# Kernel optimization log

Measured on AMD Instinct MI355X. Metric: run time of the kernel, lower is better.

## Reference

```python
import jax, jax.numpy as jnp
import numpy as np

C_IN, SEQ_LEN, K, G = 12, 8192, 8, 64
DIVISOR = 2 if G > 1 else 1
_G = G // DIVISOR
MAX_EXP = int(np.log2((SEQ_LEN - 1) / (9 - 1)))
DILATIONS = [2 ** e for e in range(MAX_EXP + 1)]   # 10 dilations for seq_len=8192
PADDINGS = [(9 - 1) * d // 2 for d in DILATIONS]
C_IN_PER = int(np.clip(C_IN // 2, 2, 8))
BATCH = 32


def _normalize(W):
    # zero-mean, L1-normalized over the kernel taps (last dim)
    W = W - W.mean(-1, keepdims=True)
    return W / jnp.abs(W).sum(-1, keepdims=True)


def setup_inputs() -> dict:
    key = jax.random.key(0)
    kx, kw, ki = jax.random.split(key, 3)
    X = jax.random.normal(kx, (BATCH, C_IN, SEQ_LEN), dtype=jnp.float32)
    # W: (num_dilations, divisor, k*_g, 1, 9) grouped-conv kernels
    W = _normalize(jax.random.normal(kw, (len(DILATIONS), DIVISOR, K * _G, 1, 9), dtype=jnp.float32))
    # I: (num_dilations, divisor, _g, c_in_per) channel-gather indices
    I = jax.random.randint(ki, (len(DILATIONS), DIVISOR, _G, C_IN_PER), 0, C_IN)
    return {"X": X, "W": W, "I": I}


def _branch(inp, Wd, d, p):
    # inp: (bs, _G, L); Wd: (K*_G, 1, 9); grouped dilated conv, 1 in-ch -> K out-ch per group
    z = jax.lax.conv_general_dilated(
        inp, Wd, window_strides=(1,), padding=[(p, p)], rhs_dilation=(d,),
        dimension_numbers=("NCH", "OIH", "NCH"), feature_group_count=_G)
    bs = inp.shape[0]
    z = z.reshape(bs, _G, K, -1)                      # (bs, _G, K, L)
    max_vals = z.max(axis=2)                          # (bs, _G, L)
    max_idx = z.argmax(axis=2)
    min_idx = z.argmin(axis=2)
    # histogram over K bins: sum of max values at argmax bin; count at argmin bin
    cmax = jnp.stack([jnp.where(max_idx == i, max_vals, 0.0).sum(-1) for i in range(K)], axis=-1)
    cmin = jnp.stack([(min_idx == i).astype(inp.dtype).sum(-1) for i in range(K)], axis=-1)
    return cmax, cmin                                 # each (bs, _G, K)


def reference(X, W, I):
    diff_X = jnp.diff(X, axis=-1)
    Z = []
    for di, (d, p) in enumerate(zip(DILATIONS, PADDINGS)):
        for j in range(min(2, G)):
            src = X if j == 0 else diff_X
            inp = src[:, I[di, j]].sum(2)             # gather channels, sum -> (bs, _G, L)
            cmax, cmin = _branch(inp, W[di, j], d, p)
            Z.append(cmax)
            Z.append(cmin)
    Z = jnp.concatenate(Z, axis=1)                    # (bs, 4*num_dilations*_G, K)
    return jax.nn.relu(Z)
```

## Files before the change

kernel.cpp:

```cpp
#include <hip/hip_runtime.h>


typedef __fp16 h2_t __attribute__((ext_vector_type(2)));

#define NB    32
#define CIN   12
#define SEQ   8192
#define NG    32
#define CPER  6
#define OUTCH 1280
#define XS_FLOATS 7728
#define GRID  10240

#define MAX3F(a, b, c) ({ float _r; asm("v_max3_f32 %0, %1, %2, %3" \
    : "=v"(_r) : "v"(a), "v"(b), "v"(c)); _r; })
#define MIN3F(a, b, c) ({ float _r; asm("v_min3_f32 %0, %1, %2, %3" \
    : "=v"(_r) : "v"(a), "v"(b), "v"(c)); _r; })

template <int DI>
__device__ __forceinline__ void hydra_body(
    const float* __restrict__ X, const float* __restrict__ W,
    const int* __restrict__ I, float* __restrict__ out,
    float* Xs, float* Smx, int j, int b, int chunk) {

  constexpr int d   = 1 << DI;
  constexpr int R   = (d < 16) ? d : 16;
  constexpr int rb  = (DI < 4) ? DI : 4;
  constexpr int Mm  = SEQ / d;
  constexpr int TMc = 512 / R;
  constexpr int TM  = (TMc < Mm) ? TMc : Mm;
  constexpr int MC  = Mm / TM;
  constexpr int RC  = d / R;
  constexpr int NR  = (RC * MC) / 16;
  constexpr int SR  = TM + 8;
  constexpr int CS  = R * SR + 4;
  constexpr int CL  = (R >= 8) ? TM : (TM * R / 8);
  constexpr int REP = (R == 16) ? 2 : 1;

  const int L = SEQ - j;
  const int tid = threadIdx.x;
  const int g = tid >> 3, s = tid & 7;

  h2_t Wp[8][4];
  float Wt[8];
  {
    const float* wp = W + (size_t)((DI * 2 + j) * 256 + g * 8) * 9;
#pragma unroll
    for (int k = 0; k < 8; ++k) {
#pragma unroll
      for (int t = 0; t < 4; ++t)
        Wp[k][t] = __builtin_amdgcn_cvt_pkrtz(wp[k * 9 + 2 * t], wp[k * 9 + 2 * t + 1]);
      Wt[k] = wp[k * 9 + 8];
    }
  }
  const float* base[CPER];
  {
    const int* ip = I + ((DI * 2 + j) * NG + g) * CPER;
#pragma unroll
    for (int i = 0; i < CPER; ++i) base[i] = Xs + ip[i] * CS;
  }

#pragma unroll
  for (int k = 0; k < 8; ++k) Smx[k * 256 + tid] = 0.f;

  unsigned long long cmnp = 0ull;

  for (int n = 0; n < NR; ++n) {
    const int cidx = chunk + 16 * n;
    const int rc = cidx & (RC - 1);
    const int mc = cidx / RC;
    const int r0 = rc * R;
    const int m0 = mc * TM;

    if (NR > 1 && n) __syncthreads();

    {
      const float* xb0 = X + (size_t)b * CIN * SEQ;
      if (j == 0) {
        for (int f = tid; f < R * SR; f += 256) {
          int rr = f & (R - 1), mm = f >> rb, mp = m0 + mm - 4;
          int pos = r0 + rr + mp * d;
          bool ok = (mp >= 0) && (pos < L);
          int lo = rr * SR + mm;
          const float* xp = xb0 + pos;
#pragma unroll
          for (int ch = 0; ch < CIN; ++ch) {
            Xs[ch * CS + lo] = ok ? xp[0] : 0.f;
            xp += SEQ;
          }
        }
      } else {
        for (int f = tid; f < R * SR; f += 256) {
          int rr = f & (R - 1), mm = f >> rb, mp = m0 + mm - 4;
          int pos = r0 + rr + mp * d;
          bool ok = (mp >= 0) && (pos < L);
          int lo = rr * SR + mm;
          const float* xp = xb0 + pos;
#pragma unroll
          for (int ch = 0; ch < CIN; ++ch) {
            Xs[ch * CS + lo] = ok ? (xp[1] - xp[0]) : 0.f;
            xp += SEQ;
          }
        }
      }
    }
    __syncthreads();

#pragma unroll
    for (int rep = 0; rep < REP; ++rep) {
      int rr = (R == 16) ? (s + (rep << 3)) : (s & (R - 1));
      int mst = (R >= 8) ? 0 : ((s >> rb) * CL);
      int rowoff = rr * SR + mst;

      auto ldsum = [&](int idx) {
        float4 r = *reinterpret_cast<const float4*>(base[0] + idx);
#pragma unroll
        for (int i = 1; i < CPER; ++i) {
          float4 t = *reinterpret_cast<const float4*>(base[i] + idx);
          r.x += t.x; r.y += t.y; r.z += t.z; r.w += t.w;
        }
        return r;
      };

      float4 w0 = ldsum(rowoff);
      float4 w1 = ldsum(rowoff + 4);
#pragma unroll 1
      for (int st = 0; st < CL; st += 8) {
        float4 w2 = ldsum(rowoff + st + 8);
        float4 w3 = ldsum(rowoff + st + 12);
        float xv[16] = {w0.x, w0.y, w0.z, w0.w,
                        w1.x, w1.y, w1.z, w1.w,
                        w2.x, w2.y, w2.z, w2.w,
                        w3.x, w3.y, w3.z, w3.w};
        h2_t E[8], O[7];
#pragma unroll
        for (int i = 0; i < 8; ++i)
          E[i] = __builtin_amdgcn_cvt_pkrtz(xv[2 * i], xv[2 * i + 1]);
#pragma unroll
        for (int i = 0; i < 7; ++i)
          O[i] = __builtin_amdgcn_cvt_pkrtz(xv[2 * i + 1], xv[2 * i + 2]);
#pragma unroll
        for (int p = 0; p < 8; ++p) {
          const h2_t* P = (p & 1) ? (O + (p >> 1)) : (E + (p >> 1));
          float tail = xv[8 + p];
          float zp[8];
#pragma unroll
          for (int k = 0; k < 8; ++k) {
            float acc = Wt[k] * tail;
            acc = __builtin_amdgcn_fdot2(Wp[k][3], P[3], acc, false);
            acc = __builtin_amdgcn_fdot2(Wp[k][2], P[2], acc, false);
            acc = __builtin_amdgcn_fdot2(Wp[k][1], P[1], acc, false);
            acc = __builtin_amdgcn_fdot2(Wp[k][0], P[0], acc, false);
            zp[k] = __uint_as_float((__float_as_uint(acc) & 0xFFFFFFF8u) | (unsigned)k);
          }
          float t1 = MAX3F(zp[0], zp[1], zp[2]);
          float t2 = MAX3F(zp[3], zp[4], zp[5]);
          float t3 = MAX3F(zp[6], zp[7], t1);
          float mxp = fmaxf(t2, t3);
          float u1 = MIN3F(zp[0], zp[1], zp[2]);
          float u2 = MIN3F(zp[3], zp[4], zp[5]);
          float u3 = MIN3F(zp[6], zp[7], u1);
          float mnp = fminf(u2, u3);
          unsigned mxb = __float_as_uint(mxp);
          Smx[((mxb & 7u) << 8) + tid] += mxp;
          unsigned mnb = __float_as_uint(mnp);
          cmnp += 1ull << ((mnb & 7u) << 3);
        }
        w0 = w2; w1 = w3;
      }
    }
  }

  __syncthreads();

  {
    int cbase = (DI * 2 + j) * 64;
    float sum = 0.f;
#pragma unroll
    for (int s2 = 0; s2 < 8; ++s2) sum += Smx[(s << 8) + (g << 3) + s2];
    atomicAdd(out + ((size_t)b * OUTCH + cbase + g) * 8 + s, sum);

    int cnts[8];
#pragma unroll
    for (int k = 0; k < 8; ++k) cnts[k] = (int)((cmnp >> (k * 8)) & 0xFFull);
#pragma unroll
    for (int k = 0; k < 8; ++k) {
#pragma unroll
      for (int off = 1; off < 8; off <<= 1)
        cnts[k] += __shfl_xor(cnts[k], off);
    }
    int vn = cnts[0];
#pragma unroll
    for (int k = 1; k < 8; ++k) vn = (s == k) ? cnts[k] : vn;
    atomicAdd(out + ((size_t)b * OUTCH + cbase + 32 + g) * 8 + s, (float)vn);
  }
}

__global__ __launch_bounds__(256, 3) void hydra_fused(
    const float* __restrict__ X, const float* __restrict__ W,
    const int* __restrict__ I, float* __restrict__ out) {
  __shared__ float Xs[XS_FLOATS];
  __shared__ float Smx[2048];
  int u = blockIdx.x;
  int dj = u % 20;
  int rest = u / 20;
  int b = rest & 31;
  int chunk = rest >> 5;
  int j = dj & 1;
  switch (dj >> 1) {
    case 0: hydra_body<0>(X, W, I, out, Xs, Smx, j, b, chunk); break;
    case 1: hydra_body<1>(X, W, I, out, Xs, Smx, j, b, chunk); break;
    case 2: hydra_body<2>(X, W, I, out, Xs, Smx, j, b, chunk); break;
    case 3: hydra_body<3>(X, W, I, out, Xs, Smx, j, b, chunk); break;
    case 4: hydra_body<4>(X, W, I, out, Xs, Smx, j, b, chunk); break;
    case 5: hydra_body<5>(X, W, I, out, Xs, Smx, j, b, chunk); break;
    case 6: hydra_body<6>(X, W, I, out, Xs, Smx, j, b, chunk); break;
    case 7: hydra_body<7>(X, W, I, out, Xs, Smx, j, b, chunk); break;
    case 8: hydra_body<8>(X, W, I, out, Xs, Smx, j, b, chunk); break;
    case 9: hydra_body<9>(X, W, I, out, Xs, Smx, j, b, chunk); break;
  }
}

__global__ void hydra_relu(float* __restrict__ out, int n) {
  int i = blockIdx.x * 256 + threadIdx.x;
  if (i < n) out[i] = fmaxf(out[i], 0.f);
}

extern "C" void kernel_launch(void* const* d_in, const int* in_sizes, int n_in,
                              void* d_out, int out_size, void* d_ws, size_t ws_size,
                              hipStream_t stream) {
  const float* X = (const float*)d_in[0];
  const float* W = (const float*)d_in[1];
  const int*   I = (const int*)d_in[2];
  float* out = (float*)d_out;

  (void)hipMemsetAsync(d_out, 0, (size_t)out_size * sizeof(float), stream);
  hydra_fused<<<GRID, 256, 0, stream>>>(X, W, I, out);
  hydra_relu<<<(out_size + 255) / 256, 256, 0, stream>>>(out, out_size);
}
```

Baseline: 421.5 us.

## Stage inputs in fp16 shared memory and fold the ninth tap into fdot2

The shared-memory staging buffer now holds fp16 values instead of fp32. Each thread converts and writes two positions at once as a packed half pair, and the channel gather-sum is done with 8-wide half vector adds. Even/odd packed pairs come from bit shifts instead of cvt_pkrtz, and the ninth tap becomes a fifth fdot2 with a zero-padded weight. The aim is to halve LDS footprint and traffic, drop conversion instructions, and allow more blocks per CU (launch bounds raised from 3 to 5). The channel sum is now accumulated in fp16, which loses more precision than the fp32 sum it replaces.

```diff
diff --git a/kernel.cpp b/kernel.cpp
--- a/kernel.cpp
+++ b/kernel.cpp
@@ -2,6 +2,7 @@
 
 
 typedef __fp16 h2_t __attribute__((ext_vector_type(2)));
+typedef __fp16 h8_t __attribute__((ext_vector_type(8)));
 
 #define NB    32
 #define CIN   12
@@ -9,7 +10,7 @@
 #define NG    32
 #define CPER  6
 #define OUTCH 1280
-#define XS_FLOATS 7728
+#define XS_H  7776
 #define GRID  10240
 
 #define MAX3F(a, b, c) ({ float _r; asm("v_max3_f32 %0, %1, %2, %3" \
@@ -21,7 +22,7 @@
 __device__ __forceinline__ void hydra_body(
     const float* __restrict__ X, const float* __restrict__ W,
     const int* __restrict__ I, float* __restrict__ out,
-    float* Xs, float* Smx, int j, int b, int chunk) {
+    __fp16* Xs, float* Smx, int j, int b, int chunk) {
 
   constexpr int d   = 1 << DI;
   constexpr int R   = (d < 16) ? d : 16;
@@ -33,7 +34,7 @@
   constexpr int RC  = d / R;
   constexpr int NR  = (RC * MC) / 16;
   constexpr int SR  = TM + 8;
-  constexpr int CS  = R * SR + 4;
+  constexpr int CS  = R * SR + 8;
   constexpr int CL  = (R >= 8) ? TM : (TM * R / 8);
   constexpr int REP = (R == 16) ? 2 : 1;
 
@@ -41,8 +42,7 @@
   const int tid = threadIdx.x;
   const int g = tid >> 3, s = tid & 7;
 
-  h2_t Wp[8][4];
-  float Wt[8];
+  h2_t Wp[8][5];
   {
     const float* wp = W + (size_t)((DI * 2 + j) * 256 + g * 8) * 9;
 #pragma unroll
@@ -50,10 +50,10 @@
 #pragma unroll
       for (int t = 0; t < 4; ++t)
         Wp[k][t] = __builtin_amdgcn_cvt_pkrtz(wp[k * 9 + 2 * t], wp[k * 9 + 2 * t + 1]);
-      Wt[k] = wp[k * 9 + 8];
-    }
-  }
-  const float* base[CPER];
+      Wp[k][4] = __builtin_amdgcn_cvt_pkrtz(wp[k * 9 + 8], 0.f);
+    }
+  }
+  const __fp16* base[CPER];
   {
     const int* ip = I + ((DI * 2 + j) * NG + g) * CPER;
 #pragma unroll
@@ -77,28 +77,38 @@
     {
       const float* xb0 = X + (size_t)b * CIN * SEQ;
       if (j == 0) {
-        for (int f = tid; f < R * SR; f += 256) {
-          int rr = f & (R - 1), mm = f >> rb, mp = m0 + mm - 4;
+        for (int f = tid; f < R * SR / 2; f += 256) {
+          int rr = f & (R - 1), mm = (f >> rb) << 1;
+          int mp = m0 + mm - 4;
           int pos = r0 + rr + mp * d;
-          bool ok = (mp >= 0) && (pos < L);
+          bool ok0 = (mp >= 0) && (pos < L);
+          bool ok1 = (mp >= -1) && (pos + d < L);
           int lo = rr * SR + mm;
           const float* xp = xb0 + pos;
 #pragma unroll
           for (int ch = 0; ch < CIN; ++ch) {
-            Xs[ch * CS + lo] = ok ? xp[0] : 0.f;
+            float v0 = ok0 ? xp[0] : 0.f;
+            float v1 = ok1 ? xp[d] : 0.f;
+            *reinterpret_cast<h2_t*>(&Xs[ch * CS + lo]) =
+                __builtin_amdgcn_cvt_pkrtz(v0, v1);
             xp += SEQ;
           }
         }
       } else {
-        for (int f = tid; f < R * SR; f += 256) {
-          int rr = f & (R - 1), mm = f >> rb, mp = m0 + mm - 4;
+        for (int f = tid; f < R * SR / 2; f += 256) {
+          int rr = f & (R - 1), mm = (f >> rb) << 1;
+          int mp = m0 + mm - 4;
           int pos = r0 + rr + mp * d;
-          bool ok = (mp >= 0) && (pos < L);
+          bool ok0 = (mp >= 0) && (pos < L);
+          bool ok1 = (mp >= -1) && (pos + d < L);
           int lo = rr * SR + mm;
           const float* xp = xb0 + pos;
 #pragma unroll
           for (int ch = 0; ch < CIN; ++ch) {
-            Xs[ch * CS + lo] = ok ? (xp[1] - xp[0]) : 0.f;
+            float v0 = ok0 ? (xp[1] - xp[0]) : 0.f;
+            float v1 = ok1 ? (xp[d + 1] - xp[d]) : 0.f;
+            *reinterpret_cast<h2_t*>(&Xs[ch * CS + lo]) =
+                __builtin_amdgcn_cvt_pkrtz(v0, v1);
             xp += SEQ;
           }
         }
@@ -113,40 +123,34 @@
       int rowoff = rr * SR + mst;
 
       auto ldsum = [&](int idx) {
-        float4 r = *reinterpret_cast<const float4*>(base[0] + idx);
-#pragma unroll
-        for (int i = 1; i < CPER; ++i) {
-          float4 t = *reinterpret_cast<const float4*>(base[i] + idx);
-          r.x += t.x; r.y += t.y; r.z += t.z; r.w += t.w;
-        }
+        h8_t r = *reinterpret_cast<const h8_t*>(base[0] + idx);
+#pragma unroll
+        for (int i = 1; i < CPER; ++i)
+          r += *reinterpret_cast<const h8_t*>(base[i] + idx);
         return r;
       };
 
-      float4 w0 = ldsum(rowoff);
-      float4 w1 = ldsum(rowoff + 4);
+      h8_t w0 = ldsum(rowoff);
 #pragma unroll 1
       for (int st = 0; st < CL; st += 8) {
-        float4 w2 = ldsum(rowoff + st + 8);
-        float4 w3 = ldsum(rowoff + st + 12);
-        float xv[16] = {w0.x, w0.y, w0.z, w0.w,
-                        w1.x, w1.y, w1.z, w1.w,
-                        w2.x, w2.y, w2.z, w2.w,
-                        w3.x, w3.y, w3.z, w3.w};
-        h2_t E[8], O[7];
-#pragma unroll
-        for (int i = 0; i < 8; ++i)
-          E[i] = __builtin_amdgcn_cvt_pkrtz(xv[2 * i], xv[2 * i + 1]);
+        h8_t w1 = ldsum(rowoff + st + 8);
+        uint4 u0 = __builtin_bit_cast(uint4, w0);
+        uint4 u1 = __builtin_bit_cast(uint4, w1);
+        unsigned int e[8] = {u0.x, u0.y, u0.z, u0.w, u1.x, u1.y, u1.z, u1.w};
+        h2_t Eh[8], Oh[8];
+#pragma unroll
+        for (int i = 0; i < 8; ++i) Eh[i] = __builtin_bit_cast(h2_t, e[i]);
 #pragma unroll
         for (int i = 0; i < 7; ++i)
-          O[i] = __builtin_amdgcn_cvt_pkrtz(xv[2 * i + 1], xv[2 * i + 2]);
+          Oh[i] = __builtin_bit_cast(h2_t, (e[i] >> 16) | (e[i + 1] << 16));
+        Oh[7] = __builtin_bit_cast(h2_t, e[7] >> 16);
 #pragma unroll
         for (int p = 0; p < 8; ++p) {
-          const h2_t* P = (p & 1) ? (O + (p >> 1)) : (E + (p >> 1));
-          float tail = xv[8 + p];
+          const h2_t* P = (p & 1) ? (Oh + (p >> 1)) : (Eh + (p >> 1));
           float zp[8];
 #pragma unroll
           for (int k = 0; k < 8; ++k) {
-            float acc = Wt[k] * tail;
+            float acc = __builtin_amdgcn_fdot2(Wp[k][4], P[4], 0.f, false);
             acc = __builtin_amdgcn_fdot2(Wp[k][3], P[3], acc, false);
             acc = __builtin_amdgcn_fdot2(Wp[k][2], P[2], acc, false);
             acc = __builtin_amdgcn_fdot2(Wp[k][1], P[1], acc, false);
@@ -157,16 +161,16 @@
           float t2 = MAX3F(zp[3], zp[4], zp[5]);
           float t3 = MAX3F(zp[6], zp[7], t1);
           float mxp = fmaxf(t2, t3);
-          float u1 = MIN3F(zp[0], zp[1], zp[2]);
-          float u2 = MIN3F(zp[3], zp[4], zp[5]);
-          float u3 = MIN3F(zp[6], zp[7], u1);
-          float mnp = fminf(u2, u3);
+          float u1v = MIN3F(zp[0], zp[1], zp[2]);
+          float u2v = MIN3F(zp[3], zp[4], zp[5]);
+          float u3v = MIN3F(zp[6], zp[7], u1v);
+          float mnp = fminf(u2v, u3v);
           unsigned mxb = __float_as_uint(mxp);
           Smx[((mxb & 7u) << 8) + tid] += mxp;
           unsigned mnb = __float_as_uint(mnp);
           cmnp += 1ull << ((mnb & 7u) << 3);
         }
-        w0 = w2; w1 = w3;
+        w0 = w1;
       }
     }
   }
@@ -196,10 +200,10 @@
   }
 }
 
-__global__ __launch_bounds__(256, 3) void hydra_fused(
+__global__ __launch_bounds__(256, 5) void hydra_fused(
     const float* __restrict__ X, const float* __restrict__ W,
     const int* __restrict__ I, float* __restrict__ out) {
-  __shared__ float Xs[XS_FLOATS];
+  __shared__ __fp16 Xs[XS_H];
   __shared__ float Smx[2048];
   int u = blockIdx.x;
   int dj = u % 20;
```

Measured after the change: 452.6 us. 7.4% more time.
